# Performance work log

Measured on AMD Instinct MI355X. Metric: run time of the kernel, lower is better.

Reference implementation:

```python
import jax, jax.numpy as jnp
import numpy as np
from jax.ops import segment_sum, segment_max

N = 400000          # points
V = 100000          # occupied voxels
EPS = 1e-3          # BN eps from norm_cfg
VX, VY, VZ = 0.2, 0.2, 4.0          # voxel_size
X0, Y0, Z0 = 0.0, -40.0, -3.0       # point_cloud_range mins
GX, GY, GZ = 352, 400, 1            # grid dims


def setup_inputs() -> dict:
    key = jax.random.key(0)
    ks = jax.random.split(key, 12)
    # points: xyz uniform inside the point cloud range, 4th channel = intensity
    xyz = jax.random.uniform(ks[0], (N, 3), jnp.float32) \
        * jnp.array([70.4, 80.0, 4.0], jnp.float32) \
        + jnp.array([X0, Y0, Z0], jnp.float32)
    inten = jax.random.uniform(ks[1], (N, 1), jnp.float32)
    features = jnp.concatenate([xyz, inten], axis=1)
    # point -> voxel mapping; guarantee every voxel id occupied so
    # segment_max semantics match torch's unique-voxel reduce exactly
    inv = jnp.concatenate([jnp.arange(V, dtype=jnp.int32),
                           jax.random.randint(ks[2], (N - V,), 0, V, jnp.int32)])
    inv = jax.random.permutation(ks[3], inv)
    # voxel coordinates (batch, z, y, x)
    b = jax.random.randint(ks[4], (V,), 0, 2, jnp.int32)
    z = jnp.zeros((V,), jnp.int32)
    y = jax.random.randint(ks[5], (V,), 0, GY, jnp.int32)
    x = jax.random.randint(ks[6], (V,), 0, GX, jnp.int32)
    coors = jnp.stack([b, z, y, x], axis=1)
    # VFE params: Linear(bias=False) + BN1d(gamma, beta)
    W0 = jax.random.normal(ks[7], (64, 10), jnp.float32) * (1.0 / np.sqrt(10))
    W1 = jax.random.normal(ks[8], (64, 128), jnp.float32) * (1.0 / np.sqrt(128))
    return dict(features=features, W0=W0,
                gamma0=jnp.ones((64,), jnp.float32), beta0=jnp.zeros((64,), jnp.float32),
                W1=W1,
                gamma1=jnp.ones((64,), jnp.float32), beta1=jnp.zeros((64,), jnp.float32),
                inv=inv, coors=coors)


def _bn_relu(x, gamma, beta):
    # BN1d in training mode: biased batch stats over the point dim
    mu = jnp.mean(x, axis=0)
    var = jnp.var(x, axis=0)
    return jax.nn.relu(gamma * (x - mu) * jax.lax.rsqrt(var + EPS) + beta)


def _stats(xyz, inv, coors):
    # cluster-center offset: per-voxel mean of xyz, gathered back
    cnt = segment_sum(jnp.ones((xyz.shape[0],), xyz.dtype), inv, num_segments=V)
    mean = segment_sum(xyz, inv, num_segments=V) / cnt[:, None]
    f_cluster = xyz - mean[inv]
    # voxel-center offset: coors order is (batch, z, y, x)
    cf = coors.astype(xyz.dtype)
    center = jnp.stack([cf[:, 3] * VX + VX / 2 + X0,
                        cf[:, 2] * VY + VY / 2 + Y0,
                        cf[:, 1] * VZ + VZ / 2 + Z0], axis=1)
    f_center = xyz - center[inv]
    return jnp.concatenate([xyz, f_cluster, f_center], axis=1)  # [N, 9]


def reference(features, W0, gamma0, beta0, W1, gamma1, beta1, inv, coors):
    x = jnp.concatenate([_stats(features[:, :3], inv, coors), features[:, 3:]], axis=1)  # [N,10]
    # VFE layer 0
    h0 = _bn_relu(x @ W0.T, gamma0, beta0)                     # [N,64]
    v0 = segment_max(h0, inv, num_segments=V)                  # [V,64]
    x1 = jnp.concatenate([h0, v0[inv]], axis=1)                # [N,128]
    # VFE layer 1
    h1 = _bn_relu(x1 @ W1.T, gamma1, beta1)                    # [N,64]
    voxel_feats = segment_max(h1, inv, num_segments=V)         # [V,64]
    return voxel_feats, coors
```

## Files before the change

kernel.cpp:

```cpp
#include <hip/hip_runtime.h>
#include <hip/hip_bf16.h>

#define NPTS 400000
#define NVOX 100000
#define EPSB 1e-3f
#define NTILE 6250
#define NBLK_SCAN 391
#define GBLK 782

#define OFF_ACC4   0
#define OFF_GRAM   (4*NVOX)
#define OFF_P1     (OFF_GRAM + 128)
#define ZERO_FLOATS (OFF_P1 + 4096)
#define OFF_Y1M    ZERO_FLOATS
#define OFF_VTMP   (OFF_Y1M + NVOX*64)
#define OFF_BSUM   (OFF_VTMP + NVOX)
#define OFF_VOFF   (OFF_BSUM + 512)
#define OFF_VSTART (OFF_VOFF + NVOX)
#define OFF_ORD    (OFF_VSTART + NVOX + 8)
#define OFF_VS     (OFF_ORD + NPTS)
#define OFF_W0F    (OFF_VS + NPTS)
#define OFF_W1B    (OFF_W0F + 640)

#define XTB_LD 136
#define HT_LD  65

typedef __bf16 bf16x8 __attribute__((ext_vector_type(8)));
typedef float  f32x4  __attribute__((ext_vector_type(4)));

__device__ __forceinline__ float b2f(__hip_bfloat16 h) { return __bfloat162float(h); }
__device__ __forceinline__ float bfbits2f(unsigned short u) {
    return __uint_as_float((unsigned int)u << 16);
}
__device__ __forceinline__ unsigned short bf16u(float f) {
    __hip_bfloat16 h = __float2bfloat16(f);
    return __builtin_bit_cast(unsigned short, h);
}
__device__ __forceinline__ unsigned int fkey(float f) {
    unsigned int u = __float_as_uint(f);
    return (u & 0x80000000u) ? ~u : (u | 0x80000000u);
}
__device__ __forceinline__ float funkey(unsigned int k) {
    unsigned int u = (k & 0x80000000u) ? (k & 0x7FFFFFFFu) : ~k;
    return __uint_as_float(u);
}

__device__ __forceinline__ void compute_x(const __hip_bfloat16* __restrict__ feat,
                                          const float* __restrict__ acc4,
                                          const int* __restrict__ coors,
                                          long i, int v, float* xv) {
    ushort4 f4 = *(const ushort4*)(feat + 4 * i);
    float px = bfbits2f(f4.x), py = bfbits2f(f4.y), pz = bfbits2f(f4.z), it = bfbits2f(f4.w);
    float4 a4 = *(const float4*)&acc4[4 * (long)v];
    float ic = 1.0f / a4.x;
    int4 c4 = *(const int4*)&coors[4 * (long)v];
    xv[0] = px; xv[1] = py; xv[2] = pz;
    xv[3] = px - a4.y * ic; xv[4] = py - a4.z * ic; xv[5] = pz - a4.w * ic;
    xv[6] = px - ((float)c4.w * 0.2f + 0.1f);
    xv[7] = py - ((float)c4.z * 0.2f + 0.1f - 40.0f);
    xv[8] = pz - ((float)c4.y * 4.0f + 2.0f - 3.0f);
    xv[9] = it;
}

__global__ void k_vsum(const __hip_bfloat16* __restrict__ feat,
                       const int* __restrict__ inv,
                       float* __restrict__ acc4,
                       const __hip_bfloat16* __restrict__ W0,
                       const __hip_bfloat16* __restrict__ W1,
                       float* __restrict__ W0f, unsigned short* __restrict__ w1b) {
    if (blockIdx.x == 6250) {
        int t = threadIdx.x;
        for (int j = t; j < 640; j += 256) W0f[j] = b2f(W0[j]);
        for (int f = t; f < 8192; f += 256) {
            int j  = f & 7;
            int l  = (f >> 3) & 63;
            int ks = (f >> 9) & 3;
            int ct = f >> 11;
            int ch = ct * 16 + (l & 15);
            int k  = ks * 32 + ((l >> 4) & 3) * 8 + j;
            w1b[f] = __builtin_bit_cast(unsigned short, W1[ch * 128 + k]);
        }
        return;
    }
    long t = (long)blockIdx.x * 256 + threadIdx.x;
    int pt = (int)(t >> 2);
    int comp = (int)(t & 3);
    float val = (comp == 0) ? 1.0f : b2f(feat[4 * pt + comp - 1]);
    int v = inv[pt];
    atomicAdd(&acc4[(long)v * 4 + comp], val);
}

__global__ void k_scan1(const float* __restrict__ acc4,
                        int* __restrict__ vtmp, int* __restrict__ bsum) {
    __shared__ int sc[256];
    int b = blockIdx.x, t = threadIdx.x;
    int v = b * 256 + t;
    int c = (v < NVOX) ? (int)acc4[4 * (long)v] : 0;
    sc[t] = c;
    __syncthreads();
    int val = c;
    for (int off = 1; off < 256; off <<= 1) {
        int x = (t >= off) ? sc[t - off] : 0;
        __syncthreads();
        val += x; sc[t] = val;
        __syncthreads();
    }
    if (v < NVOX) vtmp[v] = val - c;
    if (t == 255) bsum[b] = val;
}

__global__ void k_scan2(int* __restrict__ bsum) {
    __shared__ int sc[512];
    int t = threadIdx.x;
    int c = (t < NBLK_SCAN) ? bsum[t] : 0;
    sc[t] = c;
    __syncthreads();
    int val = c;
    for (int off = 1; off < 512; off <<= 1) {
        int x = (t >= off) ? sc[t - off] : 0;
        __syncthreads();
        val += x; sc[t] = val;
        __syncthreads();
    }
    if (t < NBLK_SCAN) bsum[t] = val - c;
}

__global__ void k_scan3(const int* __restrict__ vtmp, const int* __restrict__ bsum,
                        int* __restrict__ voff, int* __restrict__ vstart,
                        unsigned int* __restrict__ y1m) {
    int v = blockIdx.x * 256 + threadIdx.x;
    if (v < NVOX) {
        int s0 = vtmp[v] + bsum[v >> 8];
        voff[v] = s0;
        vstart[v] = s0;
        int s1;
        if (v + 1 < NVOX) s1 = vtmp[v + 1] + bsum[(v + 1) >> 8];
        else              s1 = NPTS;
        if ((s0 >> 4) != ((s1 - 1) >> 4)) {
            float4 z4 = {0.f, 0.f, 0.f, 0.f};
            float4* py = (float4*)&y1m[(long)v * 64];
#pragma unroll
            for (int u = 0; u < 16; u++) py[u] = z4;
        }
    }
    if (v == 0) vstart[NVOX] = NPTS;
}

__global__ __launch_bounds__(256, 4)
void k_prep(const __hip_bfloat16* __restrict__ feat,
            const int* __restrict__ inv,
            const int* __restrict__ coors,
            const float* __restrict__ acc4,
            int* __restrict__ voff,
            int* __restrict__ ord, int* __restrict__ vsorted,
            float* __restrict__ gram) {
    __shared__ float gs[72];
    int t = threadIdx.x;
    if (t < 72) gs[t] = 0.0f;
    __syncthreads();

    float sx[10], sxx[55];
#pragma unroll
    for (int a = 0; a < 10; a++) sx[a] = 0.0f;
#pragma unroll
    for (int a = 0; a < 55; a++) sxx[a] = 0.0f;

    for (long i = (long)blockIdx.x * 256 + t; i < NPTS; i += (long)GBLK * 256) {
        int v = inv[i];
        float xv[10];
        compute_x(feat, acc4, coors, i, v, xv);
        int idx = 0;
#pragma unroll
        for (int a = 0; a < 10; a++) {
            sx[a] += xv[a];
#pragma unroll
            for (int b = 0; b <= a; b++) sxx[idx++] += xv[a] * xv[b];
        }
        int pos = atomicAdd(&voff[v], 1);
        ord[pos] = (int)i;
        vsorted[pos] = v;
    }

#pragma unroll
    for (int v = 0; v < 65; v++) {
        float s = (v < 10) ? sx[v] : sxx[v - 10];
        for (int m = 32; m >= 1; m >>= 1) s += __shfl_xor(s, m);
        if ((t & 63) == 0) atomicAdd(&gs[v], s);
    }
    __syncthreads();
    if (t < 65) atomicAdd(&gram[t], gs[t]);
}

__global__ __launch_bounds__(256, 4)
void k_fused(const int* __restrict__ ord, const int* __restrict__ vsorted,
             const int* __restrict__ vstart,
             const __hip_bfloat16* __restrict__ feat,
             const float* __restrict__ acc4, const int* __restrict__ coors,
             const float* __restrict__ W0f, const float* __restrict__ gram,
             const __hip_bfloat16* __restrict__ g0,
             const __hip_bfloat16* __restrict__ be0,
             const unsigned short* __restrict__ w1b,
             float* __restrict__ P1, unsigned int* __restrict__ y1m) {
    __shared__ union {
        unsigned short xtb[64 * XTB_LD];
        float ht[64 * HT_LD];
    } sm;
    __shared__ unsigned int vms[64 * 65];
    __shared__ float xvs[640];
    __shared__ int invs[64];
    __shared__ float sc0s[64], bi0s[64];
    __shared__ int sext[2];

    int t = threadIdx.x, w = t >> 6, l = t & 63;
    int quad = l >> 4, lm = l & 15;
    int base = blockIdx.x * 64;

#pragma unroll
    for (int u = 0; u < 17; u++) {
        int idx = t + u * 256;
        if (idx < 64 * 65) vms[idx] = 0u;
    }

    if (w == 0) {
        int i = ord[base + l];
        int v = vsorted[base + l];
        invs[l] = v;
        float xv[10];
        compute_x(feat, acc4, coors, (long)i, v, xv);
#pragma unroll
        for (int k = 0; k < 10; k++) xvs[k * 64 + l] = xv[k];
        if (l == 0)  sext[0] = vstart[v];
        if (l == 63) sext[1] = vstart[v + 1];
    } else if (w == 1) {
        int c = l;
        float wr[10];
#pragma unroll
        for (int k = 0; k < 10; k++) wr[k] = W0f[c * 10 + k];
        float sum = 0.0f, sq = 0.0f;
#pragma unroll
        for (int a = 0; a < 10; a++) {
            sum += wr[a] * gram[a];
            float ta = 0.0f;
#pragma unroll
            for (int b = 0; b < 10; b++) {
                int hi = (a >= b) ? a : b, lo = (a >= b) ? b : a;
                ta += wr[b] * gram[10 + hi * (hi + 1) / 2 + lo];
            }
            sq += wr[a] * ta;
        }
        float mu  = sum * (1.0f / NPTS);
        float var = sq * (1.0f / NPTS) - mu * mu;
        float g   = b2f(g0[c]) * rsqrtf(var + EPSB);
        sc0s[c] = g;
        bi0s[c] = b2f(be0[c]) - mu * g;
    }

    bf16x8 bfrag[4];
    const uint4* wf = (const uint4*)w1b;
#pragma unroll
    for (int ks = 0; ks < 4; ks++)
        bfrag[ks] = __builtin_bit_cast(bf16x8, wf[(w * 4 + ks) * 64 + l]);

    __syncthreads();

    int v_lo = invs[0];
    int cw = w * 16;

    {
        float xv[10];
#pragma unroll
        for (int k = 0; k < 10; k++) xv[k] = xvs[k * 64 + l];
        int slot = invs[l] - v_lo;
#pragma unroll
        for (int jj = 0; jj < 8; jj++) {
            int c0 = cw + 2 * jj;
            float ya = 0.0f, yb = 0.0f;
#pragma unroll
            for (int k = 0; k < 10; k++) {
                ya += xv[k] * W0f[c0 * 10 + k];
                yb += xv[k] * W0f[(c0 + 1) * 10 + k];
            }
            float ha = fmaxf(sc0s[c0] * ya + bi0s[c0], 0.0f);
            float hb = fmaxf(sc0s[c0 + 1] * yb + bi0s[c0 + 1], 0.0f);
            unsigned int pk = (unsigned int)bf16u(ha) | ((unsigned int)bf16u(hb) << 16);
            *(unsigned int*)&sm.xtb[l * XTB_LD + c0] = pk;
            atomicMax(&vms[slot * 65 + c0],     __float_as_uint(ha));
            atomicMax(&vms[slot * 65 + c0 + 1], __float_as_uint(hb));
        }
    }

    {
        int s_lo = sext[0], s_hi = sext[1];
        int L = base - s_lo;
        int T = s_hi - (base + 64);
        int v_hi = invs[63];
        int slot_hi = v_hi - v_lo;
        for (int j0 = 0; j0 < L + T; j0 += 64) {
            int j = j0 + l;
            if (j < L + T) {
                int lead = (j < L) ? 1 : 0;
                int g  = lead ? (s_lo + j) : (base + 64 + (j - L));
                int vv = lead ? v_lo : v_hi;
                int slot = lead ? 0 : slot_hi;
                int i = ord[g];
                float xv[10];
                compute_x(feat, acc4, coors, (long)i, vv, xv);
#pragma unroll
                for (int jj = 0; jj < 16; jj++) {
                    int c = cw + jj;
                    float y = 0.0f;
#pragma unroll
                    for (int k = 0; k < 10; k++) y += xv[k] * W0f[c * 10 + k];
                    float h = fmaxf(sc0s[c] * y + bi0s[c], 0.0f);
                    atomicMax(&vms[slot * 65 + c], __float_as_uint(h));
                }
            }
        }
    }
    __syncthreads();

    {
        int p = t >> 2, q = t & 3;
        int slot = invs[p] - v_lo;
        const unsigned int* src = &vms[slot * 65 + q * 16];
#pragma unroll
        for (int u = 0; u < 4; u++) {
            ushort4 s4;
            s4.x = bf16u(__uint_as_float(src[4 * u + 0]));
            s4.y = bf16u(__uint_as_float(src[4 * u + 1]));
            s4.z = bf16u(__uint_as_float(src[4 * u + 2]));
            s4.w = bf16u(__uint_as_float(src[4 * u + 3]));
            *(ushort4*)&sm.xtb[p * XTB_LD + 64 + q * 16 + 4 * u] = s4;
        }
    }
    __syncthreads();

    f32x4 acc[4];
#pragma unroll
    for (int pg = 0; pg < 4; pg++) acc[pg] = (f32x4){0.f, 0.f, 0.f, 0.f};
#pragma unroll
    for (int ks = 0; ks < 4; ks++) {
#pragma unroll
        for (int pg = 0; pg < 4; pg++) {
            const uint4* ap = (const uint4*)&sm.xtb[(pg * 16 + lm) * XTB_LD + ks * 32 + quad * 8];
            bf16x8 a = __builtin_bit_cast(bf16x8, *ap);
            acc[pg] = __builtin_amdgcn_mfma_f32_16x16x32_bf16(a, bfrag[ks], acc[pg], 0, 0, 0);
        }
    }

    float ssum = 0.0f, ssq = 0.0f;
#pragma unroll
    for (int pg = 0; pg < 4; pg++) {
#pragma unroll
        for (int r = 0; r < 4; r++) {
            float y = acc[pg][r];
            ssum += y; ssq += y * y;
        }
    }
    __syncthreads();

#pragma unroll
    for (int pg = 0; pg < 4; pg++) {
#pragma unroll
        for (int r = 0; r < 4; r++)
            sm.ht[(pg * 16 + quad * 4 + r) * HT_LD + w * 16 + lm] = acc[pg][r];
    }
    __syncthreads();

    unsigned int mk = 0u;
#pragma unroll
    for (int j = 0; j < 16; j++) {
        int p = cw + j;
        unsigned int k2 = fkey(sm.ht[p * HT_LD + l]);
        mk = (k2 > mk) ? k2 : mk;
        if (j == 15 || invs[p + 1] != invs[p]) {
            int vv = invs[p];
            int s0 = vstart[vv], s1 = vstart[vv + 1];
            unsigned int* dst = &y1m[(long)vv * 64 + l];
            if (s0 >= base + cw && s1 <= base + cw + 16)
                *dst = mk;
            else
                atomicMax(dst, mk);
            mk = 0u;
        }
    }

    ssum += __shfl_xor(ssum, 16); ssq += __shfl_xor(ssq, 16);
    ssum += __shfl_xor(ssum, 32); ssq += __shfl_xor(ssq, 32);
    if (l < 16) {
        int slot = blockIdx.x & 31;
        atomicAdd(&P1[slot * 128 + w * 16 + lm], ssum);
        atomicAdd(&P1[slot * 128 + 64 + w * 16 + lm], ssq);
    }
}

#define OUTBLK 512
__global__ __launch_bounds__(256)
void k_out(const unsigned int* __restrict__ y1m,
           const float* __restrict__ P1,
           const __hip_bfloat16* __restrict__ gamma,
           const __hip_bfloat16* __restrict__ beta,
           const int* __restrict__ coors,
           float* __restrict__ out) {
    __shared__ float sc1s[64], bi1s[64];
    int t = threadIdx.x;
    if (t < 64) {
        float sum = 0.0f, sq = 0.0f;
        for (int s = 0; s < 32; s++) {
            sum += P1[s*128 + t];
            sq  += P1[s*128 + 64 + t];
        }
        float mu  = sum * (1.0f / NPTS);
        float var = sq * (1.0f / NPTS) - mu * mu;
        float g   = b2f(gamma[t]) * rsqrtf(var + EPSB);
        sc1s[t] = g;
        bi1s[t] = b2f(beta[t]) - mu * g;
    }
    __syncthreads();

    const long n4feat = (long)NVOX * 16;
    const long n4all  = n4feat + NVOX;
    const long nfeat  = (long)NVOX * 64;
    for (long idx = (long)blockIdx.x * 256 + t; idx < n4all; idx += (long)OUTBLK * 256) {
        if (idx < n4feat) {
            uint4 kk = ((const uint4*)y1m)[idx];
            int c0 = (int)((idx * 4) & 63);
            float4 o;
            o.x = fmaxf(sc1s[c0+0] * funkey(kk.x) + bi1s[c0+0], 0.0f);
            o.y = fmaxf(sc1s[c0+1] * funkey(kk.y) + bi1s[c0+1], 0.0f);
            o.z = fmaxf(sc1s[c0+2] * funkey(kk.z) + bi1s[c0+2], 0.0f);
            o.w = fmaxf(sc1s[c0+3] * funkey(kk.w) + bi1s[c0+3], 0.0f);
            ((float4*)out)[idx] = o;
        } else {
            long vi = idx - n4feat;
            int4 c4 = ((const int4*)coors)[vi];
            float4 o;
            o.x = b2f(__float2bfloat16((float)c4.x));
            o.y = b2f(__float2bfloat16((float)c4.y));
            o.z = b2f(__float2bfloat16((float)c4.z));
            o.w = b2f(__float2bfloat16((float)c4.w));
            ((float4*)(out + nfeat))[vi] = o;
        }
    }
}

extern "C" void kernel_launch(void* const* d_in, const int* in_sizes, int n_in,
                              void* d_out, int out_size, void* d_ws, size_t ws_size,
                              hipStream_t stream) {
    const __hip_bfloat16* feat = (const __hip_bfloat16*)d_in[0];
    const __hip_bfloat16* W0   = (const __hip_bfloat16*)d_in[1];
    const __hip_bfloat16* g0   = (const __hip_bfloat16*)d_in[2];
    const __hip_bfloat16* be0  = (const __hip_bfloat16*)d_in[3];
    const __hip_bfloat16* W1   = (const __hip_bfloat16*)d_in[4];
    const __hip_bfloat16* g1   = (const __hip_bfloat16*)d_in[5];
    const __hip_bfloat16* be1  = (const __hip_bfloat16*)d_in[6];
    const int* inv   = (const int*)d_in[7];
    const int* coors = (const int*)d_in[8];
    float* out = (float*)d_out;

    float* ws    = (float*)d_ws;
    float* acc4  = ws + OFF_ACC4;
    float* gram  = ws + OFF_GRAM;
    float* P1    = ws + OFF_P1;
    unsigned int* y1m = (unsigned int*)(ws + OFF_Y1M);
    int* vtmp    = (int*)(ws + OFF_VTMP);
    int* bsum    = (int*)(ws + OFF_BSUM);
    int* voff    = (int*)(ws + OFF_VOFF);
    int* vstart  = (int*)(ws + OFF_VSTART);
    int* ord     = (int*)(ws + OFF_ORD);
    int* vsorted = (int*)(ws + OFF_VS);
    float* W0f   = ws + OFF_W0F;
    unsigned short* w1b = (unsigned short*)(ws + OFF_W1B);

    hipMemsetAsync(ws, 0, (size_t)ZERO_FLOATS * sizeof(float), stream);

    k_vsum<<<6251, 256, 0, stream>>>(feat, inv, acc4, W0, W1, W0f, w1b);
    k_scan1<<<NBLK_SCAN, 256, 0, stream>>>(acc4, vtmp, bsum);
    k_scan2<<<1, 512, 0, stream>>>(bsum);
    k_scan3<<<NBLK_SCAN, 256, 0, stream>>>(vtmp, bsum, voff, vstart, y1m);
    k_prep<<<GBLK, 256, 0, stream>>>(feat, inv, coors, acc4, voff, ord, vsorted, gram);
    k_fused<<<NTILE, 256, 0, stream>>>(ord, vsorted, vstart, feat, acc4, coors,
                                       W0f, gram, g0, be0, w1b, P1, y1m);
    k_out<<<OUTBLK, 256, 0, stream>>>(y1m, P1, g1, be1, coors, out);
}
```

Before: 276.4 us.

## Replace per-slot shared atomic max table with sorted segmented scan over bf16 rows

Removes the 64x65 shared-memory max table and its per-element atomicMax calls. Because the points in each block are sorted by voxel, the per-voxel max is now computed by a sequential scan over the bf16 rows already held in shared memory. Each wave writes the result only for its own 16 rows, and boundary voxels that span neighbouring blocks are handled through a small 128-entry atomic buffer. The smaller LDS footprint lets launch bounds be raised from 4 to 6 blocks per CU. The cost is a serial 64-step loop per thread and taking the max on bf16 bit patterns instead of fp32, which is valid here because all values are non-negative after ReLU.

```diff
diff --git a/kernel.cpp b/kernel.cpp
--- a/kernel.cpp
+++ b/kernel.cpp
@@ -191,7 +191,7 @@
     if (t < 65) atomicAdd(&gram[t], gs[t]);
 }
 
-__global__ __launch_bounds__(256, 4)
+__global__ __launch_bounds__(256, 6)
 void k_fused(const int* __restrict__ ord, const int* __restrict__ vsorted,
              const int* __restrict__ vstart,
              const __hip_bfloat16* __restrict__ feat,
@@ -205,21 +205,17 @@
         unsigned short xtb[64 * XTB_LD];
         float ht[64 * HT_LD];
     } sm;
-    __shared__ unsigned int vms[64 * 65];
     __shared__ float xvs[640];
     __shared__ int invs[64];
     __shared__ float sc0s[64], bi0s[64];
+    __shared__ unsigned int bnd[128];
     __shared__ int sext[2];
 
     int t = threadIdx.x, w = t >> 6, l = t & 63;
     int quad = l >> 4, lm = l & 15;
     int base = blockIdx.x * 64;
 
-#pragma unroll
-    for (int u = 0; u < 17; u++) {
-        int idx = t + u * 256;
-        if (idx < 64 * 65) vms[idx] = 0u;
-    }
+    if (t < 128) bnd[t] = 0u;
 
     if (w == 0) {
         int i = ord[base + l];
@@ -263,14 +259,13 @@
 
     __syncthreads();
 
-    int v_lo = invs[0];
     int cw = w * 16;
 
     {
         float xv[10];
 #pragma unroll
         for (int k = 0; k < 10; k++) xv[k] = xvs[k * 64 + l];
-        int slot = invs[l] - v_lo;
+        unsigned int pk[8];
 #pragma unroll
         for (int jj = 0; jj < 8; jj++) {
             int c0 = cw + 2 * jj;
@@ -282,26 +277,26 @@
             }
             float ha = fmaxf(sc0s[c0] * ya + bi0s[c0], 0.0f);
             float hb = fmaxf(sc0s[c0 + 1] * yb + bi0s[c0 + 1], 0.0f);
-            unsigned int pk = (unsigned int)bf16u(ha) | ((unsigned int)bf16u(hb) << 16);
-            *(unsigned int*)&sm.xtb[l * XTB_LD + c0] = pk;
-            atomicMax(&vms[slot * 65 + c0],     __float_as_uint(ha));
-            atomicMax(&vms[slot * 65 + c0 + 1], __float_as_uint(hb));
-        }
+            pk[jj] = (unsigned int)bf16u(ha) | ((unsigned int)bf16u(hb) << 16);
+        }
+        uint4 u0 = {pk[0], pk[1], pk[2], pk[3]};
+        uint4 u1 = {pk[4], pk[5], pk[6], pk[7]};
+        *(uint4*)&sm.xtb[l * XTB_LD + cw] = u0;
+        *(uint4*)&sm.xtb[l * XTB_LD + cw + 8] = u1;
     }
 
     {
         int s_lo = sext[0], s_hi = sext[1];
         int L = base - s_lo;
         int T = s_hi - (base + 64);
-        int v_hi = invs[63];
-        int slot_hi = v_hi - v_lo;
+        int v_lo = invs[0], v_hi = invs[63];
         for (int j0 = 0; j0 < L + T; j0 += 64) {
             int j = j0 + l;
             if (j < L + T) {
                 int lead = (j < L) ? 1 : 0;
                 int g  = lead ? (s_lo + j) : (base + 64 + (j - L));
                 int vv = lead ? v_lo : v_hi;
-                int slot = lead ? 0 : slot_hi;
+                unsigned int* bd = &bnd[lead ? 0 : 64];
                 int i = ord[g];
                 float xv[10];
                 compute_x(feat, acc4, coors, (long)i, vv, xv);
@@ -312,7 +307,7 @@
 #pragma unroll
                     for (int k = 0; k < 10; k++) y += xv[k] * W0f[c * 10 + k];
                     float h = fmaxf(sc0s[c] * y + bi0s[c], 0.0f);
-                    atomicMax(&vms[slot * 65 + c], __float_as_uint(h));
+                    atomicMax(&bd[c], (unsigned int)bf16u(h));
                 }
             }
         }
@@ -320,17 +315,20 @@
     __syncthreads();
 
     {
-        int p = t >> 2, q = t & 3;
-        int slot = invs[p] - v_lo;
-        const unsigned int* src = &vms[slot * 65 + q * 16];
-#pragma unroll
-        for (int u = 0; u < 4; u++) {
-            ushort4 s4;
-            s4.x = bf16u(__uint_as_float(src[4 * u + 0]));
-            s4.y = bf16u(__uint_as_float(src[4 * u + 1]));
-            s4.z = bf16u(__uint_as_float(src[4 * u + 2]));
-            s4.w = bf16u(__uint_as_float(src[4 * u + 3]));
-            *(ushort4*)&sm.xtb[p * XTB_LD + 64 + q * 16 + 4 * u] = s4;
+        unsigned int vmax = 0u;
+        int p0 = 0;
+        for (int p = 0; p < 64; p++) {
+            unsigned int hb = sm.xtb[p * XTB_LD + l];
+            vmax = (hb > vmax) ? hb : vmax;
+            if (p == 63 || invs[p + 1] != invs[p]) {
+                if (p0 == 0) { unsigned int b0 = bnd[l];      vmax = (b0 > vmax) ? b0 : vmax; }
+                if (p == 63) { unsigned int b1 = bnd[64 + l]; vmax = (b1 > vmax) ? b1 : vmax; }
+                int lo = (p0 > cw) ? p0 : cw;
+                int hi = (p < cw + 15) ? p : (cw + 15);
+                for (int q = lo; q <= hi; q++)
+                    sm.xtb[q * XTB_LD + 64 + l] = (unsigned short)vmax;
+                vmax = 0u; p0 = p + 1;
+            }
         }
     }
     __syncthreads();
```

Result: slower. 304.2 us (+10.1%).
